# Optimization experiments

Measured on AMD Instinct MI355X. Metric: run time of the kernel, lower is better.

The kernel has to match this reference:

```python
import jax, jax.numpy as jnp
import numpy as np

TOKENS, D_IN, D_OUT, RANK = 16384, 4096, 4096, 512

def setup_inputs() -> dict:
    key = jax.random.key(0)
    k1, k2, k3, k4 = jax.random.split(key, 4)
    x = jax.random.normal(k1, (TOKENS, D_IN), dtype=jnp.float32)
    U = jax.random.normal(k2, (D_OUT, RANK), dtype=jnp.float32) * 0.02
    sigma = jax.random.uniform(k3, (RANK,), dtype=jnp.float32)
    V = jax.random.normal(k4, (D_IN, RANK), dtype=jnp.float32) * 0.02
    return {"x": x, "U": U, "sigma": sigma, "V": V}

def reference(x, U, sigma, V):
    # W = U @ diag(sigma) @ V.T  (shape [out, in]); out = x @ W.T
    # diag(sigma) contraction expressed as a column scale of U (same math).
    W = (U * sigma[None, :]) @ V.T          # [out, in]
    return x @ W.T                          # [tokens, out]
```

## Files before the change

### kernel.cpp

```cpp
#include <hip/hip_runtime.h>

typedef __bf16 bf16;
typedef __bf16 bf16x4 __attribute__((ext_vector_type(4)));
typedef __bf16 bf16x8 __attribute__((ext_vector_type(8)));
typedef float  f32x4  __attribute__((ext_vector_type(4)));

#define TOKENS 16384
#define D_IN   4096
#define D_OUT  4096
#define RANK   512

__device__ inline void gload_lds16(const bf16* g, bf16* l) {
    __builtin_amdgcn_global_load_lds((const __attribute__((address_space(1))) void*)g,
                                     (__attribute__((address_space(3))) void*)l,
                                     16, 0, 0);
}

__global__ __launch_bounds__(256) void vt_scale(const float* __restrict__ V,
                                                const float* __restrict__ sg,
                                                bf16* __restrict__ Vst) {
    __shared__ float tile[64][65];
    const int tx = threadIdx.x & 63;
    const int ty = threadIdx.x >> 6;
    const int kb = blockIdx.x * 64;
    const int rb = blockIdx.y * 64;
    const float s = sg[rb + tx];
#pragma unroll
    for (int i = ty; i < 64; i += 4)
        tile[i][tx] = V[(size_t)(kb + i) * RANK + rb + tx] * s;
    __syncthreads();
#pragma unroll
    for (int i = ty; i < 64; i += 4)
        Vst[(size_t)(rb + i) * D_IN + kb + tx] = (bf16)tile[tx][i];
}

__global__ __launch_bounds__(256) void cvt_bf16_4(const float* __restrict__ in,
                                                  bf16* __restrict__ o, int n4) {
    int i = blockIdx.x * 256 + threadIdx.x;
    if (i < n4) {
        f32x4 v = *(const f32x4*)(in + (size_t)i * 4);
        bf16x4 b = { (bf16)v[0], (bf16)v[1], (bf16)v[2], (bf16)v[3] };
        *(bf16x4*)(o + (size_t)i * 4) = b;
    }
}

template <bool A_F32, bool OUT_BF16>
__global__ __launch_bounds__(256) void gemm_bt(const void* __restrict__ A_,
                                               const bf16* __restrict__ B,
                                               void* __restrict__ out_,
                                               int M, int N, int K) {
    __shared__ bf16 Al[128 * 64];
    __shared__ bf16 Bl[128 * 64];

    const int t  = threadIdx.x;
    const int l  = t & 63;
    const int w  = t >> 6;
    const int wr = w >> 1, wc = w & 1;
    const int lr = l & 15;
    const int kg = l >> 4;

    const int nwg = gridDim.x;
    const int bid = blockIdx.x;
    const int cpx = nwg >> 3;
    const int swz = (bid & 7) * cpx + (bid >> 3);
    const int ntn = N >> 7;
    const int tm  = (swz / ntn) << 7;
    const int tn  = (swz % ntn) << 7;

    f32x4 acc[4][4] = {};

    for (int kt = 0; kt < K; kt += 64) {
        if constexpr (A_F32) {
            const float* Af = (const float*)A_;
#pragma unroll
            for (int c = 0; c < 8; ++c) {
                int j = c * 256 + t;
                int row = j >> 4, cg = j & 15;
                f32x4 v = *(const f32x4*)(Af + (size_t)(tm + row) * K + kt + cg * 4);
                bf16x4 b = { (bf16)v[0], (bf16)v[1], (bf16)v[2], (bf16)v[3] };
                *(bf16x4*)&Al[row * 64 + cg * 4] = b;
            }
        } else {
            const bf16* Ab = (const bf16*)A_;
#pragma unroll
            for (int c = 0; c < 4; ++c) {
                int i = c * 256 + t;
                int row = i >> 3, g8 = i & 7;
                gload_lds16(Ab + (size_t)(tm + row) * K + kt + g8 * 8, &Al[i * 8]);
            }
        }
#pragma unroll
        for (int c = 0; c < 4; ++c) {
            int i = c * 256 + t;
            int row = i >> 3, g8 = i & 7;
            gload_lds16(B + (size_t)(tn + row) * K + kt + g8 * 8, &Bl[i * 8]);
        }
        __syncthreads();

#pragma unroll
        for (int ks = 0; ks < 2; ++ks) {
            bf16x8 af[4], bfr[4];
#pragma unroll
            for (int f = 0; f < 4; ++f) {
                af[f]  = *(const bf16x8*)&Al[(wr * 64 + f * 16 + lr) * 64 + ks * 32 + kg * 8];
                bfr[f] = *(const bf16x8*)&Bl[(wc * 64 + f * 16 + lr) * 64 + ks * 32 + kg * 8];
            }
#pragma unroll
            for (int fm = 0; fm < 4; ++fm)
#pragma unroll
                for (int fn = 0; fn < 4; ++fn)
                    acc[fm][fn] = __builtin_amdgcn_mfma_f32_16x16x32_bf16(
                        af[fm], bfr[fn], acc[fm][fn], 0, 0, 0);
        }
        __syncthreads();
    }

    const int r0 = tm + wr * 64 + kg * 4;
    const int c0 = tn + wc * 64 + lr;
#pragma unroll
    for (int fm = 0; fm < 4; ++fm)
#pragma unroll
        for (int fn = 0; fn < 4; ++fn)
#pragma unroll
            for (int r = 0; r < 4; ++r) {
                size_t idx = (size_t)(r0 + fm * 16 + r) * N + (c0 + fn * 16);
                if constexpr (OUT_BF16) ((bf16*)out_)[idx]  = (bf16)acc[fm][fn][r];
                else                    ((float*)out_)[idx] = acc[fm][fn][r];
            }
}

extern "C" void kernel_launch(void* const* d_in, const int* in_sizes, int n_in,
                              void* d_out, int out_size, void* d_ws, size_t ws_size,
                              hipStream_t stream) {
    const float* x  = (const float*)d_in[0];
    const float* U  = (const float*)d_in[1];
    const float* sg = (const float*)d_in[2];
    const float* V  = (const float*)d_in[3];
    float* out = (float*)d_out;

    char* ws = (char*)d_ws;
    bf16* Vst = (bf16*)ws;
    bf16* Ub  = (bf16*)(ws + (4u << 20));
    bf16* T   = (bf16*)(ws + (8u << 20));

    vt_scale<<<dim3(D_IN / 64, RANK / 64), 256, 0, stream>>>(V, sg, Vst);
    cvt_bf16_4<<<(D_OUT * RANK / 4 + 255) / 256, 256, 0, stream>>>(U, Ub, D_OUT * RANK / 4);

    gemm_bt<true, true><<<(TOKENS / 128) * (RANK / 128), 256, 0, stream>>>(
        x, Vst, T, TOKENS, RANK, D_IN);

    gemm_bt<false, false><<<(TOKENS / 128) * (D_OUT / 128), 256, 0, stream>>>(
        T, Ub, out, TOKENS, D_OUT, RANK);
}
```

Before: 275.8 us.

## Replace LDS-staged GEMM with register-direct loads and software double-buffering

Both GEMMs stop staging tiles through shared memory. Each wave now loads its MFMA fragments straight from global memory into registers, and a two-stage register double buffer overlaps the next tile's loads with the current MFMAs. This removes the LDS writes and reads and the two barriers per K-step. In exchange, each wave loads its A and B rows without sharing them across waves, which doubles redundant global or L2 traffic. The fragment loads are narrow strided 16-byte reads, and the extra buffers raise register pressure, which may lower occupancy.

```diff
diff --git a/kernel.cpp b/kernel.cpp
--- a/kernel.cpp
+++ b/kernel.cpp
@@ -9,12 +9,6 @@
 #define D_IN   4096
 #define D_OUT  4096
 #define RANK   512
-
-__device__ inline void gload_lds16(const bf16* g, bf16* l) {
-    __builtin_amdgcn_global_load_lds((const __attribute__((address_space(1))) void*)g,
-                                     (__attribute__((address_space(3))) void*)l,
-                                     16, 0, 0);
-}
 
 __global__ __launch_bounds__(256) void vt_scale(const float* __restrict__ V,
                                                 const float* __restrict__ sg,
@@ -44,20 +38,25 @@
     }
 }
 
-template <bool A_F32, bool OUT_BF16>
-__global__ __launch_bounds__(256) void gemm_bt(const void* __restrict__ A_,
-                                               const bf16* __restrict__ B,
-                                               void* __restrict__ out_,
-                                               int M, int N, int K) {
-    __shared__ bf16 Al[128 * 64];
-    __shared__ bf16 Bl[128 * 64];
+__device__ inline bf16x8 cvt8(f32x4 a, f32x4 b) {
+    bf16x8 r;
+    r[0] = (bf16)a[0]; r[1] = (bf16)a[1]; r[2] = (bf16)a[2]; r[3] = (bf16)a[3];
+    r[4] = (bf16)b[0]; r[5] = (bf16)b[1]; r[6] = (bf16)b[2]; r[7] = (bf16)b[3];
+    return r;
+}
 
+template <bool AF32, bool OUTBF16>
+__global__ __launch_bounds__(256) void gemm_flat(const void* __restrict__ A_,
+                                                 const bf16* __restrict__ B,
+                                                 void* __restrict__ out_,
+                                                 int M, int N, int K) {
     const int t  = threadIdx.x;
     const int l  = t & 63;
     const int w  = t >> 6;
     const int wr = w >> 1, wc = w & 1;
     const int lr = l & 15;
     const int kg = l >> 4;
+    const int kme = kg * 8;
 
     const int nwg = gridDim.x;
     const int bid = blockIdx.x;
@@ -67,52 +66,72 @@
     const int tm  = (swz / ntn) << 7;
     const int tn  = (swz % ntn) << 7;
 
+    const float* Af = (const float*)A_;
+    const bf16*  Ab = (const bf16*)A_;
+
+    size_t aoff[4], boff[4];
+#pragma unroll
+    for (int f = 0; f < 4; ++f) {
+        aoff[f] = (size_t)(tm + wr * 64 + f * 16 + lr) * K;
+        boff[f] = (size_t)(tn + wc * 64 + f * 16 + lr) * K;
+    }
+
     f32x4 acc[4][4] = {};
 
-    for (int kt = 0; kt < K; kt += 64) {
-        if constexpr (A_F32) {
-            const float* Af = (const float*)A_;
-#pragma unroll
-            for (int c = 0; c < 8; ++c) {
-                int j = c * 256 + t;
-                int row = j >> 4, cg = j & 15;
-                f32x4 v = *(const f32x4*)(Af + (size_t)(tm + row) * K + kt + cg * 4);
-                bf16x4 b = { (bf16)v[0], (bf16)v[1], (bf16)v[2], (bf16)v[3] };
-                *(bf16x4*)&Al[row * 64 + cg * 4] = b;
-            }
-        } else {
-            const bf16* Ab = (const bf16*)A_;
-#pragma unroll
-            for (int c = 0; c < 4; ++c) {
-                int i = c * 256 + t;
-                int row = i >> 3, g8 = i & 7;
-                gload_lds16(Ab + (size_t)(tm + row) * K + kt + g8 * 8, &Al[i * 8]);
-            }
+    f32x4  sa32[4][2][2];
+    bf16x8 afr[4][2];
+    bf16x8 sa0[4][2], sa1[4][2];
+    bf16x8 sb0[4][2], sb1[4][2];
+
+#define LD_B(SB, KT)                                                          \
+    _Pragma("unroll") for (int f = 0; f < 4; ++f)                             \
+    _Pragma("unroll") for (int ks = 0; ks < 2; ++ks)                          \
+        SB[f][ks] = *(const bf16x8*)(B + boff[f] + (KT) + ks * 32 + kme);
+
+#define LD_A32(KT)                                                            \
+    _Pragma("unroll") for (int f = 0; f < 4; ++f)                             \
+    _Pragma("unroll") for (int ks = 0; ks < 2; ++ks)                          \
+    _Pragma("unroll") for (int h = 0; h < 2; ++h)                             \
+        sa32[f][ks][h] = *(const f32x4*)(Af + aoff[f] + (KT) + ks * 32 + kme + h * 4);
+
+#define CVT_A()                                                               \
+    _Pragma("unroll") for (int f = 0; f < 4; ++f)                             \
+    _Pragma("unroll") for (int ks = 0; ks < 2; ++ks)                          \
+        afr[f][ks] = cvt8(sa32[f][ks][0], sa32[f][ks][1]);
+
+#define LD_A16(SA, KT)                                                        \
+    _Pragma("unroll") for (int f = 0; f < 4; ++f)                             \
+    _Pragma("unroll") for (int ks = 0; ks < 2; ++ks)                          \
+        SA[f][ks] = *(const bf16x8*)(Ab + aoff[f] + (KT) + ks * 32 + kme);
+
+#define COMPUTE(AF, SB)                                                       \
+    _Pragma("unroll") for (int ks = 0; ks < 2; ++ks)                          \
+    _Pragma("unroll") for (int fm = 0; fm < 4; ++fm)                          \
+    _Pragma("unroll") for (int fn = 0; fn < 4; ++fn)                          \
+        acc[fm][fn] = __builtin_amdgcn_mfma_f32_16x16x32_bf16(                \
+            AF[fm][ks], SB[fn][ks], acc[fm][fn], 0, 0, 0);
+
+    const int NT = K >> 6;
+
+    if constexpr (AF32) {
+        LD_A32(0); LD_B(sb0, 0);
+        CVT_A();
+        for (int i = 0; i < NT; i += 2) {
+            LD_A32((i + 1) * 64); LD_B(sb1, (i + 1) * 64);
+            COMPUTE(afr, sb0);
+            CVT_A();
+            if (i + 2 < NT) { LD_A32((i + 2) * 64); LD_B(sb0, (i + 2) * 64); }
+            COMPUTE(afr, sb1);
+            if (i + 2 < NT) CVT_A();
         }
-#pragma unroll
-        for (int c = 0; c < 4; ++c) {
-            int i = c * 256 + t;
-            int row = i >> 3, g8 = i & 7;
-            gload_lds16(B + (size_t)(tn + row) * K + kt + g8 * 8, &Bl[i * 8]);
+    } else {
+        LD_A16(sa0, 0); LD_B(sb0, 0);
+        for (int i = 0; i < NT; i += 2) {
+            LD_A16(sa1, (i + 1) * 64); LD_B(sb1, (i + 1) * 64);
+            COMPUTE(sa0, sb0);
+            if (i + 2 < NT) { LD_A16(sa0, (i + 2) * 64); LD_B(sb0, (i + 2) * 64); }
+            COMPUTE(sa1, sb1);
         }
-        __syncthreads();
-
-#pragma unroll
-        for (int ks = 0; ks < 2; ++ks) {
-            bf16x8 af[4], bfr[4];
-#pragma unroll
-            for (int f = 0; f < 4; ++f) {
-                af[f]  = *(const bf16x8*)&Al[(wr * 64 + f * 16 + lr) * 64 + ks * 32 + kg * 8];
-                bfr[f] = *(const bf16x8*)&Bl[(wc * 64 + f * 16 + lr) * 64 + ks * 32 + kg * 8];
-            }
-#pragma unroll
-            for (int fm = 0; fm < 4; ++fm)
-#pragma unroll
-                for (int fn = 0; fn < 4; ++fn)
-                    acc[fm][fn] = __builtin_amdgcn_mfma_f32_16x16x32_bf16(
-                        af[fm], bfr[fn], acc[fm][fn], 0, 0, 0);
-        }
-        __syncthreads();
     }
 
     const int r0 = tm + wr * 64 + kg * 4;
@@ -124,9 +143,14 @@
 #pragma unroll
             for (int r = 0; r < 4; ++r) {
                 size_t idx = (size_t)(r0 + fm * 16 + r) * N + (c0 + fn * 16);
-                if constexpr (OUT_BF16) ((bf16*)out_)[idx]  = (bf16)acc[fm][fn][r];
-                else                    ((float*)out_)[idx] = acc[fm][fn][r];
+                if constexpr (OUTBF16) ((bf16*)out_)[idx]  = (bf16)acc[fm][fn][r];
+                else                   ((float*)out_)[idx] = acc[fm][fn][r];
             }
+#undef LD_B
+#undef LD_A32
+#undef CVT_A
+#undef LD_A16
+#undef COMPUTE
 }
 
 extern "C" void kernel_launch(void* const* d_in, const int* in_sizes, int n_in,
@@ -146,9 +170,9 @@
     vt_scale<<<dim3(D_IN / 64, RANK / 64), 256, 0, stream>>>(V, sg, Vst);
     cvt_bf16_4<<<(D_OUT * RANK / 4 + 255) / 256, 256, 0, stream>>>(U, Ub, D_OUT * RANK / 4);
 
-    gemm_bt<true, true><<<(TOKENS / 128) * (RANK / 128), 256, 0, stream>>>(
+    gemm_flat<true, true><<<(TOKENS / 128) * (RANK / 128), 256, 0, stream>>>(
         x, Vst, T, TOKENS, RANK, D_IN);
 
-    gemm_bt<false, false><<<(TOKENS / 128) * (D_OUT / 128), 256, 0, stream>>>(
+    gemm_flat<false, false><<<(TOKENS / 128) * (D_OUT / 128), 256, 0, stream>>>(
         T, Ub, out, TOKENS, D_OUT, RANK);
 }
```

Result: slower. 659.4 us (+139.1%).
